# Optimization experiments

Hardware: AMD Instinct MI355X
Metric: run time of the kernel (lower is better)

The kernel has to match this reference:

```python
import jax, jax.numpy as jnp
import numpy as np

N, E = 50000, 800000          # nodes, edges
F_IN, H, C = 32, 64, 7        # input feats, hidden, classes
EPS = 1e-5                    # BatchNorm eps


def setup_inputs() -> dict:
    key = jax.random.key(0)
    ks = jax.random.split(key, 16)
    inp = {
        "x": jax.random.normal(ks[0], (N, F_IN), jnp.float32),
        "edge_index": jax.random.randint(ks[1], (2, E), 0, N),
        "edge_attr": jax.random.uniform(ks[2], (E, 1), jnp.float32),
    }

    def conv_params(k, cin, cout, i):
        k1, k2 = jax.random.split(k)
        s = 1.0 / np.sqrt(cin)
        inp[f"W{i}"] = jax.random.uniform(k1, (2, cin, cout), jnp.float32, -s, s)  # spline kernel weights
        inp[f"R{i}"] = jax.random.uniform(k2, (cin, cout), jnp.float32, -s, s)     # root weight
        inp[f"B{i}"] = jnp.zeros((cout,), jnp.float32)

    conv_params(ks[3], F_IN, H, 0)
    conv_params(ks[4], H, H, 1)
    conv_params(ks[5], H, C, 2)
    for i in range(2):  # BatchNorm (eval mode: running stats)
        inp[f"G{i}"] = jnp.ones((H,), jnp.float32)
        inp[f"BE{i}"] = jnp.zeros((H,), jnp.float32)
        inp[f"RM{i}"] = 0.1 * jax.random.normal(ks[6 + 2 * i], (H,), jnp.float32)
        inp[f"RV{i}"] = jax.random.uniform(ks[7 + 2 * i], (H,), jnp.float32, 0.5, 1.5)
    return inp


def spline_conv(x, src, dst, u, W, R, B):
    # dim=1, kernel_size=2, degree=1 open B-spline:
    # basis = (1-u, u) with weight indices (0, 1) for u in [0,1).
    basis = jnp.stack([1.0 - u, u], axis=1)               # [E, 2]
    msg = jnp.einsum('ec,ek,kco->eo', x[src], basis, W)    # gather + basis-weighted linear
    agg = jax.ops.segment_sum(msg, dst, num_segments=N)    # scatter-add
    deg = jax.ops.segment_sum(jnp.ones((src.shape[0],), x.dtype), dst, num_segments=N)
    agg = agg / jnp.maximum(deg, 1.0)[:, None]             # aggr='mean' (default)
    return agg + x @ R + B                                 # root weight + bias


def batch_norm(x, g, b, rm, rv):
    return (x - rm) * jax.lax.rsqrt(rv + EPS) * g + b


def reference(x, edge_index, edge_attr,
              W0, R0, B0, W1, R1, B1, W2, R2, B2,
              G0, BE0, RM0, RV0, G1, BE1, RM1, RV1):
    src, dst = edge_index[0], edge_index[1]
    u = edge_attr[:, 0]
    h = spline_conv(x, src, dst, u, W0, R0, B0)
    h = jax.nn.elu(batch_norm(h, G0, BE0, RM0, RV0))
    h = spline_conv(h, src, dst, u, W1, R1, B1)
    h = jax.nn.elu(batch_norm(h, G1, BE1, RM1, RV1))
    h = spline_conv(h, src, dst, u, W2, R2, B2)
    return jax.nn.log_softmax(h, axis=1)
```

## Files before the change

### kernel.cpp

```cpp
#include <hip/hip_runtime.h>
#include <hip/hip_fp16.h>
#include <math.h>

#define NN 50000
#define NE 800000
#define EPSV 1e-5f
#define BSHIFT 6
#define BSIZE 64
#define NB 782
#define CAP 1408

typedef _Float16 h2f   __attribute__((ext_vector_type(2)));
typedef _Float16 f16x8 __attribute__((ext_vector_type(8)));
typedef float    f32x4 __attribute__((ext_vector_type(4)));

__global__ __launch_bounds__(64) void prep_all_kernel(
        const float* __restrict__ W0, const float* __restrict__ R0,
        const float* __restrict__ W1, const float* __restrict__ R1,
        const float* __restrict__ W2, const float* __restrict__ R2,
        const float* __restrict__ B0, const float* __restrict__ B1,
        const float* __restrict__ G0, const float* __restrict__ BE0,
        const float* __restrict__ RM0, const float* __restrict__ RV0,
        const float* __restrict__ G1, const float* __restrict__ BE1,
        const float* __restrict__ RM1, const float* __restrict__ RV1,
        __half* __restrict__ Bf0, __half* __restrict__ Bf1, __half* __restrict__ Bf7,
        float* __restrict__ bn0, float* __restrict__ bn1,
        int* __restrict__ bcursor) {
    int lane = threadIdx.x;
    int bid = blockIdx.x;
    int c = lane & 15;
    int kbase = ((lane >> 4) << 3);
    _Float16 vals[8];
    if (bid < 12) {
        int ks = bid >> 2, nt = bid & 3;
        int n = nt * 16 + c;
#pragma unroll
        for (int j = 0; j < 8; ++j) {
            int kg = ks * 32 + kbase + j;
            float v = (kg < 64) ? W0[(kg & 1) * 2048 + (kg >> 1) * 64 + n]
                                : R0[(kg - 64) * 64 + n];
            vals[j] = (_Float16)v;
        }
        *reinterpret_cast<f16x8*>(Bf0 + ((size_t)(bid * 64 + lane)) * 8) =
            *reinterpret_cast<f16x8*>(vals);
    } else if (bid < 36) {
        int t = bid - 12;
        int ks = t >> 2, nt = t & 3;
        int n = nt * 16 + c;
#pragma unroll
        for (int j = 0; j < 8; ++j) {
            int kg = ks * 32 + kbase + j;
            float v = (kg < 128) ? W1[(kg & 1) * 4096 + (kg >> 1) * 64 + n]
                                 : R1[(kg - 128) * 64 + n];
            vals[j] = (_Float16)v;
        }
        *reinterpret_cast<f16x8*>(Bf1 + ((size_t)(t * 64 + lane)) * 8) =
            *reinterpret_cast<f16x8*>(vals);
    } else if (bid < 40) {
        int ksnt = bid - 36;
        int ks = ksnt >> 1, nt = ksnt & 1;
#pragma unroll
        for (int j = 0; j < 8; ++j) {
            int k = ks * 32 + kbase + j;
            float v = 0.f;
            if (nt == 0) {
                if (c < 7)                 v = W2[k * 7 + c];
                else if (c >= 8 && c < 15) v = W2[448 + k * 7 + (c - 8)];
            } else {
                if (c < 7)                 v = R2[k * 7 + c];
            }
            vals[j] = (_Float16)v;
        }
        *reinterpret_cast<f16x8*>(Bf7 + ((size_t)(ksnt * 64 + lane)) * 8) =
            *reinterpret_cast<f16x8*>(vals);
    } else if (bid == 40) {
        float s = G0[lane] * rsqrtf(RV0[lane] + EPSV);
        bn0[lane] = s;
        bn0[64 + lane] = B0[lane] * s + BE0[lane] - RM0[lane] * s;
    } else if (bid == 41) {
        float s = G1[lane] * rsqrtf(RV1[lane] + EPSV);
        bn1[lane] = s;
        bn1[64 + lane] = B1[lane] * s + BE1[lane] - RM1[lane] * s;
    } else {
        int b = (bid - 42) * 64 + lane;
        if (b < NB) bcursor[b] = b * CAP;
    }
}

__global__ __launch_bounds__(256) void binB_xh_kernel(
        const int* __restrict__ src, const int* __restrict__ dst,
        const float* __restrict__ attr, int* __restrict__ bcursor,
        unsigned* __restrict__ es1su, unsigned char* __restrict__ es1dl, int E,
        const float* __restrict__ x, __half* __restrict__ xh) {
    __shared__ int hist[NB];
    __shared__ int base[NB];
    if (blockIdx.x >= NB) {
        int t = (blockIdx.x - NB) * 256 + threadIdx.x;
        size_t idx = (size_t)t * 8;
        if (idx < (size_t)NN * 32) {
            float4 f0 = *reinterpret_cast<const float4*>(x + idx);
            float4 f1 = *reinterpret_cast<const float4*>(x + idx + 4);
            _Float16 v[8] = {(_Float16)f0.x, (_Float16)f0.y, (_Float16)f0.z, (_Float16)f0.w,
                             (_Float16)f1.x, (_Float16)f1.y, (_Float16)f1.z, (_Float16)f1.w};
            *reinterpret_cast<f16x8*>(xh + idx) = *reinterpret_cast<f16x8*>(v);
        }
        return;
    }
    for (int i = threadIdx.x; i < NB; i += blockDim.x) hist[i] = 0;
    __syncthreads();
    const int chunk = (E + NB - 1) / NB;
    int e0 = blockIdx.x * chunk;
    int e1 = e0 + chunk; if (e1 > E) e1 = E;
    unsigned su[4]; unsigned char dlv[4]; short bv[4];
#pragma unroll
    for (int j = 0; j < 4; ++j) {
        int e = e0 + threadIdx.x + j * 256;
        if (e < e1) {
            int d = dst[e];
            int b = d >> BSHIFT;
            __half uh = __float2half_rn(attr[e]);
            su[j]  = ((unsigned)src[e] << 16) | (unsigned)__half_as_ushort(uh);
            dlv[j] = (unsigned char)(d & (BSIZE - 1));
            bv[j]  = (short)b;
            atomicAdd(&hist[b], 1);
        }
    }
    __syncthreads();
    for (int i = threadIdx.x; i < NB; i += blockDim.x) {
        int cnt = hist[i];
        base[i] = cnt ? atomicAdd(&bcursor[i], cnt) : 0;
        hist[i] = 0;
    }
    __syncthreads();
#pragma unroll
    for (int j = 0; j < 4; ++j) {
        int e = e0 + threadIdx.x + j * 256;
        if (e < e1) {
            int b = bv[j];
            int slot = base[b] + atomicAdd(&hist[b], 1);
            es1su[slot] = su[j];
            es1dl[slot] = dlv[j];
        }
    }
}

__global__ __launch_bounds__(256) void placeC_kernel(const int* __restrict__ bcursor,
                                                     const unsigned* __restrict__ es1su,
                                                     const unsigned char* __restrict__ es1dl,
                                                     int2* __restrict__ rowrange,
                                                     uint2* __restrict__ es8) {
    __shared__ int hist[BSIZE];
    __shared__ int cur[BSIZE];
    int b = blockIdx.x;
    int t = threadIdx.x;
    int bs = b * CAP;
    int be = bcursor[b];
    if (t < BSIZE) hist[t] = 0;
    __syncthreads();
    unsigned su[6]; unsigned char dlv[6];
#pragma unroll
    for (int j = 0; j < 6; ++j) {
        int i = bs + t + j * 256;
        if (i < be) {
            su[j]  = es1su[i];
            dlv[j] = es1dl[i];
            atomicAdd(&hist[dlv[j]], 1);
        }
    }
    __syncthreads();
    if (t < BSIZE) {
        int v = hist[t];
        int incl = v;
#pragma unroll
        for (int o = 1; o < 64; o <<= 1) {
            int nv = __shfl_up(incl, o, 64);
            if (t >= o) incl += nv;
        }
        int excl = incl - v;
        cur[t] = excl;
        int node = b * BSIZE + t;
        if (node < NN) {
            int2 rr; rr.x = bs + excl; rr.y = bs + excl + v;
            rowrange[node] = rr;
        }
    }
    __syncthreads();
#pragma unroll
    for (int j = 0; j < 6; ++j) {
        int i = bs + t + j * 256;
        if (i < be) {
            unsigned r = su[j];
            int dl = dlv[j];
            int slot = bs + atomicAdd(&cur[dl], 1);
            __half uh = __ushort_as_half((unsigned short)(r & 0xffffu));
            __half2 p = __halves2half2(__hsub(__ushort_as_half((unsigned short)0x3C00u), uh), uh);
            uint2 rec;
            rec.x = r >> 16;
            rec.y = *reinterpret_cast<unsigned*>(&p);
            es8[slot] = rec;
        }
    }
}

__global__ __launch_bounds__(256, 8) void gatherS32_kernel(const int2* __restrict__ rowrange,
                                                           const uint2* __restrict__ es8,
                                                           const __half* __restrict__ xh,
                                                           __half* __restrict__ S, int n_nodes) {
    int n = (blockIdx.x * blockDim.x + threadIdx.x) >> 6;
    int lane = threadIdx.x & 63;
    if (n >= n_nodes) return;
    int2 rr = rowrange[n];
    int beg = __builtin_amdgcn_readfirstlane(rr.x);
    int end = __builtin_amdgcn_readfirstlane(rr.y);
    const unsigned c2 = (unsigned)((lane & 31) << 1);
    const char* xb = (const char*)xh;
    float a0 = 0.f, a1 = 0.f, a2 = 0.f, a3 = 0.f;
    float a4 = 0.f, a5 = 0.f, a6 = 0.f, a7 = 0.f;
    float b0 = 0.f, b1 = 0.f, b2 = 0.f, b3 = 0.f;
    float b4 = 0.f, b5 = 0.f, b6 = 0.f, b7 = 0.f;
    int i = beg + (lane >> 5);
    for (; i + 14 < end; i += 16) {
        uint2 q0 = es8[i];
        uint2 q1 = es8[i + 2];
        uint2 q2 = es8[i + 4];
        uint2 q3 = es8[i + 6];
        uint2 q4 = es8[i + 8];
        uint2 q5 = es8[i + 10];
        uint2 q6 = es8[i + 12];
        uint2 q7 = es8[i + 14];
        __half x0 = *(const __half*)(xb + ((q0.x << 6) | c2));
        __half x1 = *(const __half*)(xb + ((q1.x << 6) | c2));
        __half x2 = *(const __half*)(xb + ((q2.x << 6) | c2));
        __half x3 = *(const __half*)(xb + ((q3.x << 6) | c2));
        __half x4 = *(const __half*)(xb + ((q4.x << 6) | c2));
        __half x5 = *(const __half*)(xb + ((q5.x << 6) | c2));
        __half x6 = *(const __half*)(xb + ((q6.x << 6) | c2));
        __half x7 = *(const __half*)(xb + ((q7.x << 6) | c2));
        __half2 u0 = __builtin_bit_cast(__half2, q0.y);
        __half2 u1 = __builtin_bit_cast(__half2, q1.y);
        __half2 u2 = __builtin_bit_cast(__half2, q2.y);
        __half2 u3 = __builtin_bit_cast(__half2, q3.y);
        __half2 u4 = __builtin_bit_cast(__half2, q4.y);
        __half2 u5 = __builtin_bit_cast(__half2, q5.y);
        __half2 u6 = __builtin_bit_cast(__half2, q6.y);
        __half2 u7 = __builtin_bit_cast(__half2, q7.y);
        float f0 = __half2float(x0), f1 = __half2float(x1);
        float f2 = __half2float(x2), f3 = __half2float(x3);
        float f4 = __half2float(x4), f5 = __half2float(x5);
        float f6 = __half2float(x6), f7 = __half2float(x7);
        a0 = fmaf(__low2float(u0), f0, a0); b0 = fmaf(__high2float(u0), f0, b0);
        a1 = fmaf(__low2float(u1), f1, a1); b1 = fmaf(__high2float(u1), f1, b1);
        a2 = fmaf(__low2float(u2), f2, a2); b2 = fmaf(__high2float(u2), f2, b2);
        a3 = fmaf(__low2float(u3), f3, a3); b3 = fmaf(__high2float(u3), f3, b3);
        a4 = fmaf(__low2float(u4), f4, a4); b4 = fmaf(__high2float(u4), f4, b4);
        a5 = fmaf(__low2float(u5), f5, a5); b5 = fmaf(__high2float(u5), f5, b5);
        a6 = fmaf(__low2float(u6), f6, a6); b6 = fmaf(__high2float(u6), f6, b6);
        a7 = fmaf(__low2float(u7), f7, a7); b7 = fmaf(__high2float(u7), f7, b7);
    }
    for (; i < end; i += 2) {
        uint2 q = es8[i];
        float xv = __half2float(*(const __half*)(xb + ((q.x << 6) | c2)));
        __half2 u = __builtin_bit_cast(__half2, q.y);
        a0 = fmaf(__low2float(u), xv, a0); b0 = fmaf(__high2float(u), xv, b0);
    }
    float a = ((a0 + a1) + (a2 + a3)) + ((a4 + a5) + (a6 + a7));
    float b = ((b0 + b1) + (b2 + b3)) + ((b4 + b5) + (b6 + b7));
    a += __shfl_xor(a, 32);
    b += __shfl_xor(b, 32);
    float degv = (float)(end - beg);
    if (degv < 1.f) degv = 1.f;
    float inv = 1.f / degv;
    if (lane < 32) {
        reinterpret_cast<__half2*>(S + (size_t)n * 64)[lane & 31] = __floats2half2_rn(a * inv, b * inv);
    }
}

__global__ __launch_bounds__(256, 8) void gatherS64_kernel(const int2* __restrict__ rowrange,
                                                           const uint2* __restrict__ es8,
                                                           const __half* __restrict__ ht,
                                                           __half* __restrict__ S, int n_nodes) {
    int n = (blockIdx.x * blockDim.x + threadIdx.x) >> 6;
    int lane = threadIdx.x & 63;
    if (n >= n_nodes) return;
    int2 rr = rowrange[n];
    int beg = __builtin_amdgcn_readfirstlane(rr.x);
    int end = __builtin_amdgcn_readfirstlane(rr.y);
    const unsigned c2 = (unsigned)(lane << 1);
    const char* xb = (const char*)ht;
    float a0 = 0.f, a1 = 0.f, a2 = 0.f, a3 = 0.f;
    float b0 = 0.f, b1 = 0.f, b2 = 0.f, b3 = 0.f;
    int i = beg;
    if (i < end && (i & 1)) {
        uint2 q = es8[i];
        float xv = __half2float(*(const __half*)(xb + ((q.x << 7) | c2)));
        __half2 u = __builtin_bit_cast(__half2, q.y);
        a0 = fmaf(__low2float(u), xv, a0); b0 = fmaf(__high2float(u), xv, b0);
        ++i;
    }
    for (; i + 7 < end; i += 8) {
        uint4 p0 = *reinterpret_cast<const uint4*>(es8 + i);
        uint4 p1 = *reinterpret_cast<const uint4*>(es8 + i + 2);
        uint4 p2 = *reinterpret_cast<const uint4*>(es8 + i + 4);
        uint4 p3 = *reinterpret_cast<const uint4*>(es8 + i + 6);
        __half x0 = *(const __half*)(xb + ((p0.x << 7) | c2));
        __half x1 = *(const __half*)(xb + ((p0.z << 7) | c2));
        __half x2 = *(const __half*)(xb + ((p1.x << 7) | c2));
        __half x3 = *(const __half*)(xb + ((p1.z << 7) | c2));
        __half x4 = *(const __half*)(xb + ((p2.x << 7) | c2));
        __half x5 = *(const __half*)(xb + ((p2.z << 7) | c2));
        __half x6 = *(const __half*)(xb + ((p3.x << 7) | c2));
        __half x7 = *(const __half*)(xb + ((p3.z << 7) | c2));
        __half2 u0 = __builtin_bit_cast(__half2, p0.y);
        __half2 u1 = __builtin_bit_cast(__half2, p0.w);
        __half2 u2 = __builtin_bit_cast(__half2, p1.y);
        __half2 u3 = __builtin_bit_cast(__half2, p1.w);
        __half2 u4 = __builtin_bit_cast(__half2, p2.y);
        __half2 u5 = __builtin_bit_cast(__half2, p2.w);
        __half2 u6 = __builtin_bit_cast(__half2, p3.y);
        __half2 u7 = __builtin_bit_cast(__half2, p3.w);
        float f0 = __half2float(x0), f1 = __half2float(x1);
        float f2 = __half2float(x2), f3 = __half2float(x3);
        float f4 = __half2float(x4), f5 = __half2float(x5);
        float f6 = __half2float(x6), f7 = __half2float(x7);
        a0 = fmaf(__low2float(u0), f0, a0); b0 = fmaf(__high2float(u0), f0, b0);
        a1 = fmaf(__low2float(u1), f1, a1); b1 = fmaf(__high2float(u1), f1, b1);
        a2 = fmaf(__low2float(u2), f2, a2); b2 = fmaf(__high2float(u2), f2, b2);
        a3 = fmaf(__low2float(u3), f3, a3); b3 = fmaf(__high2float(u3), f3, b3);
        a0 = fmaf(__low2float(u4), f4, a0); b0 = fmaf(__high2float(u4), f4, b0);
        a1 = fmaf(__low2float(u5), f5, a1); b1 = fmaf(__high2float(u5), f5, b1);
        a2 = fmaf(__low2float(u6), f6, a2); b2 = fmaf(__high2float(u6), f6, b2);
        a3 = fmaf(__low2float(u7), f7, a3); b3 = fmaf(__high2float(u7), f7, b3);
    }
    for (; i + 1 < end; i += 2) {
        uint4 p = *reinterpret_cast<const uint4*>(es8 + i);
        float f0 = __half2float(*(const __half*)(xb + ((p.x << 7) | c2)));
        float f1 = __half2float(*(const __half*)(xb + ((p.z << 7) | c2)));
        __half2 u0 = __builtin_bit_cast(__half2, p.y);
        __half2 u1 = __builtin_bit_cast(__half2, p.w);
        a0 = fmaf(__low2float(u0), f0, a0); b0 = fmaf(__high2float(u0), f0, b0);
        a1 = fmaf(__low2float(u1), f1, a1); b1 = fmaf(__high2float(u1), f1, b1);
    }
    if (i < end) {
        uint2 q = es8[i];
        float xv = __half2float(*(const __half*)(xb + ((q.x << 7) | c2)));
        __half2 u = __builtin_bit_cast(__half2, q.y);
        a0 = fmaf(__low2float(u), xv, a0); b0 = fmaf(__high2float(u), xv, b0);
    }
    float a = (a0 + a1) + (a2 + a3);
    float b = (b0 + b1) + (b2 + b3);
    float degv = (float)(end - beg);
    if (degv < 1.f) degv = 1.f;
    float inv = 1.f / degv;
    reinterpret_cast<__half2*>(S + (size_t)n * 128)[lane] = __floats2half2_rn(a * inv, b * inv);
}

__global__ __launch_bounds__(256) void gemmL0_kernel(const __half* __restrict__ S,
                                                     const __half* __restrict__ xh,
                                                     const __half* __restrict__ Bf0,
                                                     const float* __restrict__ bn,
                                                     __half* __restrict__ hout, int n_nodes) {
    const int lane = threadIdx.x & 63;
    const int wid  = threadIdx.x >> 6;
    int m0 = (blockIdx.x * 4 + wid) * 16;
    if (m0 >= n_nodes) return;
    f32x4 acc[4];
#pragma unroll
    for (int i = 0; i < 4; ++i) acc[i] = (f32x4){0.f, 0.f, 0.f, 0.f};
    const int arow = m0 + (lane & 15);
    const int koff = ((lane >> 4) << 3);
    const f16x8* bf = reinterpret_cast<const f16x8*>(Bf0);
    const _Float16* sp = (const _Float16*)S  + (size_t)arow * 64 + koff;
    const _Float16* xp = (const _Float16*)xh + (size_t)arow * 32 + koff;
    f16x8 a0 = *reinterpret_cast<const f16x8*>(sp);
    f16x8 a1 = *reinterpret_cast<const f16x8*>(sp + 32);
    f16x8 a2 = *reinterpret_cast<const f16x8*>(xp);
#pragma unroll
    for (int nt = 0; nt < 4; ++nt)
        acc[nt] = __builtin_amdgcn_mfma_f32_16x16x32_f16(a0, bf[nt * 64 + lane], acc[nt], 0, 0, 0);
#pragma unroll
    for (int nt = 0; nt < 4; ++nt)
        acc[nt] = __builtin_amdgcn_mfma_f32_16x16x32_f16(a1, bf[(4 + nt) * 64 + lane], acc[nt], 0, 0, 0);
#pragma unroll
    for (int nt = 0; nt < 4; ++nt)
        acc[nt] = __builtin_amdgcn_mfma_f32_16x16x32_f16(a2, bf[(8 + nt) * 64 + lane], acc[nt], 0, 0, 0);
    const int c_lo  = lane & 15;
    const int rbase = ((lane >> 4) << 2);
#pragma unroll
    for (int nt = 0; nt < 4; ++nt) {
        int cc = nt * 16 + c_lo;
        float sc = bn[cc], sh = bn[64 + cc];
#pragma unroll
        for (int r = 0; r < 4; ++r) {
            int row = m0 + rbase + r;
            if (row < n_nodes) {
                float v = acc[nt][r] * sc + sh;
                v = v > 0.f ? v : expm1f(v);
                hout[(size_t)row * 64 + cc] = __float2half(v);
            }
        }
    }
}

__global__ __launch_bounds__(256) void gemmL1_7_kernel(const __half* __restrict__ S,
                                                       const __half* __restrict__ hin,
                                                       const __half* __restrict__ Bf1,
                                                       const __half* __restrict__ Bf7,
                                                       const float* __restrict__ bn,
                                                       const float* __restrict__ Bb2,
                                                       __half* __restrict__ Yab7H,
                                                       float* __restrict__ Z7,
                                                       int n_nodes) {
    __shared__ __align__(16) char ldsH[64 * 128];
    const int lane = threadIdx.x & 63;
    const int wid  = threadIdx.x >> 6;
    int m0 = (blockIdx.x * 4 + wid) * 16;
    if (m0 >= n_nodes) return;
    f32x4 acc[4];
#pragma unroll
    for (int i = 0; i < 4; ++i) acc[i] = (f32x4){0.f, 0.f, 0.f, 0.f};
    const int arow = m0 + (lane & 15);
    const int g = lane >> 4;
    const int koff = g << 3;
    const f16x8* bf = reinterpret_cast<const f16x8*>(Bf1);
    const _Float16* sp = (const _Float16*)S   + (size_t)arow * 128 + koff;
    const _Float16* hp = (const _Float16*)hin + (size_t)arow * 64  + koff;
#pragma unroll
    for (int ks = 0; ks < 6; ++ks) {
        f16x8 av = (ks < 4) ? *reinterpret_cast<const f16x8*>(sp + ks * 32)
                            : *reinterpret_cast<const f16x8*>(hp + (ks - 4) * 32);
#pragma unroll
        for (int nt = 0; nt < 4; ++nt)
            acc[nt] = __builtin_amdgcn_mfma_f32_16x16x32_f16(av, bf[(ks * 4 + nt) * 64 + lane], acc[nt], 0, 0, 0);
    }
    const int c_lo  = lane & 15;
    const int rbase = ((lane >> 4) << 2);
#pragma unroll
    for (int nt = 0; nt < 4; ++nt) {
        int cc = nt * 16 + c_lo;
        float sc = bn[cc], sh = bn[64 + cc];
#pragma unroll
        for (int r = 0; r < 4; ++r) {
            float v = acc[nt][r] * sc + sh;
            v = v > 0.f ? v : expm1f(v);
            int rl = wid * 16 + rbase + r;
            *reinterpret_cast<__half*>(ldsH + ((rl * 128 + cc * 2) ^ ((rl & 7) << 4))) = __float2half(v);
        }
    }

    const int rowl = wid * 16 + (lane & 15);
    const int swz = (rowl & 7) << 4;
    f32x4 acc7[2];
    acc7[0] = (f32x4){0.f, 0.f, 0.f, 0.f};
    acc7[1] = (f32x4){0.f, 0.f, 0.f, 0.f};
    const f16x8* bf7 = reinterpret_cast<const f16x8*>(Bf7);
#pragma unroll
    for (int ks = 0; ks < 2; ++ks) {
        f16x8 av = *reinterpret_cast<const f16x8*>(ldsH + ((rowl * 128 + ks * 64 + g * 16) ^ swz));
#pragma unroll
        for (int nt = 0; nt < 2; ++nt)
            acc7[nt] = __builtin_amdgcn_mfma_f32_16x16x32_f16(av, bf7[(ks * 2 + nt) * 64 + lane], acc7[nt], 0, 0, 0);
    }
#pragma unroll
    for (int r = 0; r < 4; ++r) {
        int row = m0 + rbase + r;
        if (row < n_nodes) {
            if (c_lo < 7) {
                Yab7H[((size_t)row << 4) + 2 * c_lo] = __float2half(acc7[0][r]);
                Z7[((size_t)row << 3) + c_lo] = acc7[1][r] + Bb2[c_lo];
            } else if (c_lo >= 8 && c_lo < 15) {
                Yab7H[((size_t)row << 4) + 2 * (c_lo - 8) + 1] = __float2half(acc7[0][r]);
            }
        }
    }
}

__global__ void gather7_final_kernel(const int2* __restrict__ rowrange,
                                     const uint2* __restrict__ es8,
                                     const __half2* __restrict__ Yab7H,
                                     const float* __restrict__ Z7,
                                     float* __restrict__ out, int n_nodes) {
    int t = blockIdx.x * blockDim.x + threadIdx.x;
    int n = t >> 3;
    int c = t & 7;
    if (n >= n_nodes) return;
    int2 rr = rowrange[n];
    int beg = rr.x, end = rr.y;
    const unsigned c4 = (unsigned)(c << 2);
    const char* yb = (const char*)Yab7H;
    float acc0 = 0.f, acc1 = 0.f, acc2 = 0.f, acc3 = 0.f;
    if (c < 7) {
        int i = beg;
        for (; i + 7 < end; i += 8) {
            uint2 q0 = es8[i];
            uint2 q1 = es8[i + 1];
            uint2 q2 = es8[i + 2];
            uint2 q3 = es8[i + 3];
            uint2 q4 = es8[i + 4];
            uint2 q5 = es8[i + 5];
            uint2 q6 = es8[i + 6];
            uint2 q7 = es8[i + 7];
            __half2 v0 = *(const __half2*)(yb + ((q0.x << 5) | c4));
            __half2 v1 = *(const __half2*)(yb + ((q1.x << 5) | c4));
            __half2 v2 = *(const __half2*)(yb + ((q2.x << 5) | c4));
            __half2 v3 = *(const __half2*)(yb + ((q3.x << 5) | c4));
            __half2 v4 = *(const __half2*)(yb + ((q4.x << 5) | c4));
            __half2 v5 = *(const __half2*)(yb + ((q5.x << 5) | c4));
            __half2 v6 = *(const __half2*)(yb + ((q6.x << 5) | c4));
            __half2 v7 = *(const __half2*)(yb + ((q7.x << 5) | c4));
            acc0 = __builtin_amdgcn_fdot2(__builtin_bit_cast(h2f, v0), __builtin_bit_cast(h2f, q0.y), acc0, false);
            acc1 = __builtin_amdgcn_fdot2(__builtin_bit_cast(h2f, v1), __builtin_bit_cast(h2f, q1.y), acc1, false);
            acc2 = __builtin_amdgcn_fdot2(__builtin_bit_cast(h2f, v2), __builtin_bit_cast(h2f, q2.y), acc2, false);
            acc3 = __builtin_amdgcn_fdot2(__builtin_bit_cast(h2f, v3), __builtin_bit_cast(h2f, q3.y), acc3, false);
            acc0 = __builtin_amdgcn_fdot2(__builtin_bit_cast(h2f, v4), __builtin_bit_cast(h2f, q4.y), acc0, false);
            acc1 = __builtin_amdgcn_fdot2(__builtin_bit_cast(h2f, v5), __builtin_bit_cast(h2f, q5.y), acc1, false);
            acc2 = __builtin_amdgcn_fdot2(__builtin_bit_cast(h2f, v6), __builtin_bit_cast(h2f, q6.y), acc2, false);
            acc3 = __builtin_amdgcn_fdot2(__builtin_bit_cast(h2f, v7), __builtin_bit_cast(h2f, q7.y), acc3, false);
        }
        for (; i < end; ++i) {
            uint2 q = es8[i];
            __half2 v = *(const __half2*)(yb + ((q.x << 5) | c4));
            acc0 = __builtin_amdgcn_fdot2(__builtin_bit_cast(h2f, v), __builtin_bit_cast(h2f, q.y), acc0, false);
        }
    }
    float acc = (acc0 + acc1) + (acc2 + acc3);
    float degv = (float)(end - beg);
    if (degv < 1.f) degv = 1.f;
    float v = (c < 7) ? (acc / degv + Z7[(n << 3) + c]) : -1e30f;
    float m = v;
#pragma unroll
    for (int o = 1; o < 8; o <<= 1) m = fmaxf(m, __shfl_xor(m, o, 8));
    float ex = (c < 7) ? expf(v - m) : 0.f;
    float ssum = ex;
#pragma unroll
    for (int o = 1; o < 8; o <<= 1) ssum += __shfl_xor(ssum, o, 8);
    if (c < 7) out[n * 7 + c] = v - m - logf(ssum);
}

extern "C" void kernel_launch(void* const* d_in, const int* in_sizes, int n_in,
                              void* d_out, int out_size, void* d_ws, size_t ws_size,
                              hipStream_t stream) {
    const float* x    = (const float*)d_in[0];
    const int*   ei   = (const int*)d_in[1];
    const float* attr = (const float*)d_in[2];
    const float* W0 = (const float*)d_in[3];
    const float* R0 = (const float*)d_in[4];
    const float* B0 = (const float*)d_in[5];
    const float* W1 = (const float*)d_in[6];
    const float* R1 = (const float*)d_in[7];
    const float* B1 = (const float*)d_in[8];
    const float* W2 = (const float*)d_in[9];
    const float* R2 = (const float*)d_in[10];
    const float* B2 = (const float*)d_in[11];
    const float* G0  = (const float*)d_in[12];
    const float* BE0 = (const float*)d_in[13];
    const float* RM0 = (const float*)d_in[14];
    const float* RV0 = (const float*)d_in[15];
    const float* G1  = (const float*)d_in[16];
    const float* BE1 = (const float*)d_in[17];
    const float* RM1 = (const float*)d_in[18];
    const float* RV1 = (const float*)d_in[19];

    const int* src = ei;
    const int* dst = ei + NE;
    float* out = (float*)d_out;

    char* ws = (char*)d_ws;
    size_t off = 0;
    auto alloc = [&](size_t bytes) { char* p = ws + off; off += (bytes + 255) & ~size_t(255); return p; };
    int*           bcursor  = (int*)          alloc(NB * sizeof(int));
    int2*          rowrange = (int2*)         alloc((size_t)NN * sizeof(int2));
    unsigned*      es1su    = (unsigned*)     alloc((size_t)NB * CAP * sizeof(unsigned));
    unsigned char* es1dl    = (unsigned char*)alloc((size_t)NB * CAP * sizeof(unsigned char));
    uint2*         es8      = (uint2*)        alloc((size_t)NB * CAP * sizeof(uint2));
    __half*        Bf0      = (__half*)       alloc((size_t)12 * 64 * 8 * sizeof(__half));
    __half*        Bf1      = (__half*)       alloc((size_t)24 * 64 * 8 * sizeof(__half));
    __half*        Bf7      = (__half*)       alloc((size_t)4 * 64 * 8 * sizeof(__half));
    float*         bn0      = (float*)        alloc(128 * sizeof(float));
    float*         bn1      = (float*)        alloc(128 * sizeof(float));
    __half*        xh       = (__half*)       alloc((size_t)(NN + 64) * 32 * sizeof(__half));
    __half*        S        = (__half*)       alloc((size_t)(NN + 64) * 128 * sizeof(__half));
    __half*        h0       = (__half*)       alloc((size_t)(NN + 64) * 64 * sizeof(__half));
    __half*        Yab7H    = (__half*)       alloc((size_t)NN * 16 * sizeof(__half));
    float*         Z7       = (float*)        alloc((size_t)NN * 8 * sizeof(float));

    const int B = 256;
    const int gM    = ((NN + 15) / 16 + 3) / 4;
    const int gGath = (NN * 64) / B;
    const int gN8   = (NN * 8 + B - 1) / B;
    const int gConv = ((NN * 32 / 8) + B - 1) / B;
    const int gPrep = 42 + (NB + 63) / 64;

    prep_all_kernel<<<gPrep, 64, 0, stream>>>(W0, R0, W1, R1, W2, R2, B0, B1,
                                              G0, BE0, RM0, RV0, G1, BE1, RM1, RV1,
                                              Bf0, Bf1, Bf7, bn0, bn1, bcursor);

    binB_xh_kernel<<<NB + gConv, B, 0, stream>>>(src, dst, attr, bcursor, es1su, es1dl, NE, x, xh);

    placeC_kernel<<<NB, B, 0, stream>>>(bcursor, es1su, es1dl, rowrange, es8);

    gatherS32_kernel<<<gGath, B, 0, stream>>>(rowrange, es8, xh, S, NN);
    gemmL0_kernel<<<gM, B, 0, stream>>>(S, xh, Bf0, bn0, h0, NN);

    gatherS64_kernel<<<gGath, B, 0, stream>>>(rowrange, es8, h0, S, NN);
    gemmL1_7_kernel<<<gM, B, 0, stream>>>(S, h0, Bf1, Bf7, bn1, B2, Yab7H, Z7, NN);

    gather7_final_kernel<<<gN8, B, 0, stream>>>(rowrange, es8, (const __half2*)Yab7H, Z7, out, NN);
}
```

Measured before the change: 226.0 us.

## Replace two-level bucketed CSR build with global count, claim, scatter

Replaces the two-pass bucket sort (block-local histograms into fixed-capacity buckets, then per-bucket placement) with a per-node degree count using global atomics, a wavefront scan that claims contiguous ranges through one global atomic cursor, and a direct scatter that uses per-node atomic cursors. This removes the intermediate es1su/es1dl buffers and their extra write-and-read pass, and drops the fixed CAP bucket capacity. In exchange it adds one more kernel launch and relies on heavy global atomic contention on deg and cur. Row ranges are no longer in node order across wavefronts, and edge order inside a row is nondeterministic.

```diff
diff --git a/kernel.cpp b/kernel.cpp
--- a/kernel.cpp
+++ b/kernel.cpp
@@ -5,10 +5,6 @@
 #define NN 50000
 #define NE 800000
 #define EPSV 1e-5f
-#define BSHIFT 6
-#define BSIZE 64
-#define NB 782
-#define CAP 1408
 
 typedef _Float16 h2f   __attribute__((ext_vector_type(2)));
 typedef _Float16 f16x8 __attribute__((ext_vector_type(8)));
@@ -25,7 +21,7 @@
         const float* __restrict__ RM1, const float* __restrict__ RV1,
         __half* __restrict__ Bf0, __half* __restrict__ Bf1, __half* __restrict__ Bf7,
         float* __restrict__ bn0, float* __restrict__ bn1,
-        int* __restrict__ bcursor) {
+        int* __restrict__ deg, int* __restrict__ gcursor) {
     int lane = threadIdx.x;
     int bid = blockIdx.x;
     int c = lane & 15;
@@ -82,20 +78,17 @@
         bn1[lane] = s;
         bn1[64 + lane] = B1[lane] * s + BE1[lane] - RM1[lane] * s;
     } else {
-        int b = (bid - 42) * 64 + lane;
-        if (b < NB) bcursor[b] = b * CAP;
-    }
-}
-
-__global__ __launch_bounds__(256) void binB_xh_kernel(
-        const int* __restrict__ src, const int* __restrict__ dst,
-        const float* __restrict__ attr, int* __restrict__ bcursor,
-        unsigned* __restrict__ es1su, unsigned char* __restrict__ es1dl, int E,
-        const float* __restrict__ x, __half* __restrict__ xh) {
-    __shared__ int hist[NB];
-    __shared__ int base[NB];
-    if (blockIdx.x >= NB) {
-        int t = (blockIdx.x - NB) * 256 + threadIdx.x;
+        int n = (bid - 42) * 64 + lane;
+        if (n < NN) deg[n] = 0;
+        if (n == 0) *gcursor = 0;
+    }
+}
+
+__global__ __launch_bounds__(256) void count_conv_kernel(
+        const int* __restrict__ dst, int* __restrict__ deg, int E,
+        const float* __restrict__ x, __half* __restrict__ xh, int nCount) {
+    if ((int)blockIdx.x >= nCount) {
+        int t = (blockIdx.x - nCount) * 256 + threadIdx.x;
         size_t idx = (size_t)t * 8;
         if (idx < (size_t)NN * 32) {
             float4 f0 = *reinterpret_cast<const float4*>(x + idx);
@@ -106,96 +99,54 @@
         }
         return;
     }
-    for (int i = threadIdx.x; i < NB; i += blockDim.x) hist[i] = 0;
-    __syncthreads();
-    const int chunk = (E + NB - 1) / NB;
-    int e0 = blockIdx.x * chunk;
-    int e1 = e0 + chunk; if (e1 > E) e1 = E;
-    unsigned su[4]; unsigned char dlv[4]; short bv[4];
-#pragma unroll
-    for (int j = 0; j < 4; ++j) {
-        int e = e0 + threadIdx.x + j * 256;
-        if (e < e1) {
+    int e = blockIdx.x * 1024 + threadIdx.x;
+#pragma unroll
+    for (int j = 0; j < 4; ++j, e += 256) {
+        if (e < E) atomicAdd(&deg[dst[e]], 1);
+    }
+}
+
+__global__ __launch_bounds__(256) void claim_kernel(const int* __restrict__ deg,
+                                                    int* __restrict__ gcursor,
+                                                    int2* __restrict__ rowrange,
+                                                    int* __restrict__ cur, int n_nodes) {
+    int n = blockIdx.x * 256 + threadIdx.x;
+    int lane = threadIdx.x & 63;
+    int d = (n < n_nodes) ? deg[n] : 0;
+    int incl = d;
+#pragma unroll
+    for (int o = 1; o < 64; o <<= 1) {
+        int v = __shfl_up(incl, o, 64);
+        if (lane >= o) incl += v;
+    }
+    int total = __shfl(incl, 63, 64);
+    int base = 0;
+    if (lane == 63) base = atomicAdd(gcursor, total);
+    base = __shfl(base, 63, 64);
+    int beg = base + incl - d;
+    if (n < n_nodes) {
+        int2 rr; rr.x = beg; rr.y = beg + d;
+        rowrange[n] = rr;
+        cur[n] = beg;
+    }
+}
+
+__global__ __launch_bounds__(256) void scatter_kernel(const int* __restrict__ src,
+                                                      const int* __restrict__ dst,
+                                                      const float* __restrict__ attr,
+                                                      int* __restrict__ cur,
+                                                      uint2* __restrict__ es8, int E) {
+    int e = blockIdx.x * 1024 + threadIdx.x;
+#pragma unroll
+    for (int j = 0; j < 4; ++j, e += 256) {
+        if (e < E) {
             int d = dst[e];
-            int b = d >> BSHIFT;
+            int s = src[e];
             __half uh = __float2half_rn(attr[e]);
-            su[j]  = ((unsigned)src[e] << 16) | (unsigned)__half_as_ushort(uh);
-            dlv[j] = (unsigned char)(d & (BSIZE - 1));
-            bv[j]  = (short)b;
-            atomicAdd(&hist[b], 1);
-        }
-    }
-    __syncthreads();
-    for (int i = threadIdx.x; i < NB; i += blockDim.x) {
-        int cnt = hist[i];
-        base[i] = cnt ? atomicAdd(&bcursor[i], cnt) : 0;
-        hist[i] = 0;
-    }
-    __syncthreads();
-#pragma unroll
-    for (int j = 0; j < 4; ++j) {
-        int e = e0 + threadIdx.x + j * 256;
-        if (e < e1) {
-            int b = bv[j];
-            int slot = base[b] + atomicAdd(&hist[b], 1);
-            es1su[slot] = su[j];
-            es1dl[slot] = dlv[j];
-        }
-    }
-}
-
-__global__ __launch_bounds__(256) void placeC_kernel(const int* __restrict__ bcursor,
-                                                     const unsigned* __restrict__ es1su,
-                                                     const unsigned char* __restrict__ es1dl,
-                                                     int2* __restrict__ rowrange,
-                                                     uint2* __restrict__ es8) {
-    __shared__ int hist[BSIZE];
-    __shared__ int cur[BSIZE];
-    int b = blockIdx.x;
-    int t = threadIdx.x;
-    int bs = b * CAP;
-    int be = bcursor[b];
-    if (t < BSIZE) hist[t] = 0;
-    __syncthreads();
-    unsigned su[6]; unsigned char dlv[6];
-#pragma unroll
-    for (int j = 0; j < 6; ++j) {
-        int i = bs + t + j * 256;
-        if (i < be) {
-            su[j]  = es1su[i];
-            dlv[j] = es1dl[i];
-            atomicAdd(&hist[dlv[j]], 1);
-        }
-    }
-    __syncthreads();
-    if (t < BSIZE) {
-        int v = hist[t];
-        int incl = v;
-#pragma unroll
-        for (int o = 1; o < 64; o <<= 1) {
-            int nv = __shfl_up(incl, o, 64);
-            if (t >= o) incl += nv;
-        }
-        int excl = incl - v;
-        cur[t] = excl;
-        int node = b * BSIZE + t;
-        if (node < NN) {
-            int2 rr; rr.x = bs + excl; rr.y = bs + excl + v;
-            rowrange[node] = rr;
-        }
-    }
-    __syncthreads();
-#pragma unroll
-    for (int j = 0; j < 6; ++j) {
-        int i = bs + t + j * 256;
-        if (i < be) {
-            unsigned r = su[j];
-            int dl = dlv[j];
-            int slot = bs + atomicAdd(&cur[dl], 1);
-            __half uh = __ushort_as_half((unsigned short)(r & 0xffffu));
+            int slot = atomicAdd(&cur[d], 1);
             __half2 p = __halves2half2(__hsub(__ushort_as_half((unsigned short)0x3C00u), uh), uh);
             uint2 rec;
-            rec.x = r >> 16;
+            rec.x = (unsigned)s;
             rec.y = *reinterpret_cast<unsigned*>(&p);
             es8[slot] = rec;
         }
@@ -567,11 +518,11 @@
     char* ws = (char*)d_ws;
     size_t off = 0;
     auto alloc = [&](size_t bytes) { char* p = ws + off; off += (bytes + 255) & ~size_t(255); return p; };
-    int*           bcursor  = (int*)          alloc(NB * sizeof(int));
+    int*           deg      = (int*)          alloc((size_t)NN * sizeof(int));
+    int*           cur      = (int*)          alloc((size_t)NN * sizeof(int));
+    int*           gcursor  = (int*)          alloc(sizeof(int));
     int2*          rowrange = (int2*)         alloc((size_t)NN * sizeof(int2));
-    unsigned*      es1su    = (unsigned*)     alloc((size_t)NB * CAP * sizeof(unsigned));
-    unsigned char* es1dl    = (unsigned char*)alloc((size_t)NB * CAP * sizeof(unsigned char));
-    uint2*         es8      = (uint2*)        alloc((size_t)NB * CAP * sizeof(uint2));
+    uint2*         es8      = (uint2*)        alloc((size_t)(NE + 16) * sizeof(uint2));
     __half*        Bf0      = (__half*)       alloc((size_t)12 * 64 * 8 * sizeof(__half));
     __half*        Bf1      = (__half*)       alloc((size_t)24 * 64 * 8 * sizeof(__half));
     __half*        Bf7      = (__half*)       alloc((size_t)4 * 64 * 8 * sizeof(__half));
@@ -584,19 +535,21 @@
     float*         Z7       = (float*)        alloc((size_t)NN * 8 * sizeof(float));
 
     const int B = 256;
-    const int gM    = ((NN + 15) / 16 + 3) / 4;
-    const int gGath = (NN * 64) / B;
-    const int gN8   = (NN * 8 + B - 1) / B;
-    const int gConv = ((NN * 32 / 8) + B - 1) / B;
-    const int gPrep = 42 + (NB + 63) / 64;
+    const int gM     = ((NN + 15) / 16 + 3) / 4;
+    const int gGath  = (NN * 64) / B;
+    const int gN8    = (NN * 8 + B - 1) / B;
+    const int gEdge  = (NE + 1023) / 1024;
+    const int gConv  = ((NN * 32 / 8) + B - 1) / B;
+    const int gClaim = (NN + B - 1) / B;
+    const int gPrep  = 42 + (NN + 63) / 64;
 
     prep_all_kernel<<<gPrep, 64, 0, stream>>>(W0, R0, W1, R1, W2, R2, B0, B1,
                                               G0, BE0, RM0, RV0, G1, BE1, RM1, RV1,
-                                              Bf0, Bf1, Bf7, bn0, bn1, bcursor);
-
-    binB_xh_kernel<<<NB + gConv, B, 0, stream>>>(src, dst, attr, bcursor, es1su, es1dl, NE, x, xh);
-
-    placeC_kernel<<<NB, B, 0, stream>>>(bcursor, es1su, es1dl, rowrange, es8);
+                                              Bf0, Bf1, Bf7, bn0, bn1, deg, gcursor);
+
+    count_conv_kernel<<<gEdge + gConv, B, 0, stream>>>(dst, deg, NE, x, xh, gEdge);
+    claim_kernel<<<gClaim, B, 0, stream>>>(deg, gcursor, rowrange, cur, NN);
+    scatter_kernel<<<gEdge, B, 0, stream>>>(src, dst, attr, cur, es8, NE);
 
     gatherS32_kernel<<<gGath, B, 0, stream>>>(rowrange, es8, xh, S, NN);
     gemmL0_kernel<<<gM, B, 0, stream>>>(S, xh, Bf0, bn0, h0, NN);
```

Measured after the change: 286.6 us. 1.27x slower.
